# Performance work log

Measured on AMD Instinct MI355X. Metric: run time of the kernel, lower is better.

Reference implementation:

```python
import jax, jax.numpy as jnp
import numpy as np

N = 100000   # nodes per branch
E = 1600000  # edges per branch
B = 512      # graphs in batch
D = 256      # input feature dim
C = 27       # number of side-effect labels
NEG_SLOPE = 0.2


def _gat_conv(x, src, dst, W, a_src, a_dst, b):
    """PyG GATConv, heads=1, with self loops. x:[N,din], src/dst:[E+N]."""
    n = x.shape[0]
    h = x @ W                               # [N, dout]
    al_s = h @ a_src                        # [N]
    al_d = h @ a_dst                        # [N]
    e = jax.nn.leaky_relu(al_s[src] + al_d[dst], NEG_SLOPE)  # [E+N]
    # segment softmax over destination nodes (self loops guarantee non-empty)
    m = jax.ops.segment_max(e, dst, num_segments=n)
    w = jnp.exp(e - m[dst])
    denom = jax.ops.segment_sum(w, dst, num_segments=n)
    alpha = w / denom[dst]                  # [E+N]
    out = jax.ops.segment_sum(h[src] * alpha[:, None], dst, num_segments=n)
    return out + b


def _with_self_loops(edge_index, n):
    loop = jnp.arange(n, dtype=edge_index.dtype)
    src = jnp.concatenate([edge_index[0], loop])
    dst = jnp.concatenate([edge_index[1], loop])
    return src, dst


def _mean_pool(x, batch, num_graphs):
    s = jax.ops.segment_sum(x, batch, num_segments=num_graphs)
    cnt = jax.ops.segment_sum(jnp.ones(x.shape[0], x.dtype), batch, num_segments=num_graphs)
    return s / jnp.maximum(cnt, 1.0)[:, None]


def _gat_params(key, din, dout):
    k = jax.random.split(key, 4)
    sc = 1.0 / np.sqrt(din)
    return (jax.random.normal(k[0], (din, dout), jnp.float32) * sc,
            jax.random.normal(k[1], (dout,), jnp.float32) * sc,
            jax.random.normal(k[2], (dout,), jnp.float32) * sc,
            jnp.zeros((dout,), jnp.float32))


def setup_inputs() -> dict:
    key = jax.random.key(0)
    ks = jax.random.split(key, 12)
    inp = {
        'x_s': jax.random.normal(ks[0], (N, D), jnp.float32),
        'x_t': jax.random.normal(ks[1], (N, D), jnp.float32),
        'edge_index_s': jax.random.randint(ks[2], (2, E), 0, N, jnp.int32),
        'edge_index_t': jax.random.randint(ks[3], (2, E), 0, N, jnp.int32),
        'xs_batch': jnp.sort(jax.random.randint(ks[4], (N,), 0, B, jnp.int32)),
        'xt_batch': jnp.sort(jax.random.randint(ks[5], (N,), 0, B, jnp.int32)),
    }
    for name, kk, din, dout in [('s1', ks[6], D, D // 2), ('s2', ks[7], D // 2, D // 4),
                                 ('t1', ks[8], D, D // 2), ('t2', ks[9], D // 2, D // 4)]:
        W, a_s, a_d, b = _gat_params(kk, din, dout)
        inp[f'W_{name}'] = W
        inp[f'a_src_{name}'] = a_s
        inp[f'a_dst_{name}'] = a_d
        inp[f'b_{name}'] = b
    inp['lin_w'] = jax.random.normal(ks[10], (D // 4, C), jnp.float32) / np.sqrt(D // 4)
    inp['lin_b'] = jnp.zeros((C,), jnp.float32)
    return inp


def reference(x_s, x_t,
              W_s1, a_src_s1, a_dst_s1, b_s1,
              W_s2, a_src_s2, a_dst_s2, b_s2,
              W_t1, a_src_t1, a_dst_t1, b_t1,
              W_t2, a_src_t2, a_dst_t2, b_t2,
              lin_w, lin_b,
              edge_index_s, edge_index_t, xs_batch, xt_batch):
    src_s, dst_s = _with_self_loops(edge_index_s, N)
    src_t, dst_t = _with_self_loops(edge_index_t, N)

    x1 = _gat_conv(x_s, src_s, dst_s, W_s1, a_src_s1, a_dst_s1, b_s1)
    x2 = _gat_conv(x1, src_s, dst_s, W_s2, a_src_s2, a_dst_s2, b_s2)
    xs = _mean_pool(x2, xs_batch, B)

    x3 = _gat_conv(x_t, src_t, dst_t, W_t1, a_src_t1, a_dst_t1, b_t1)
    x4 = _gat_conv(x3, src_t, dst_t, W_t2, a_src_t2, a_dst_t2, b_t2)
    xt = _mean_pool(x4, xt_batch, B)

    out = (xs + xt) @ lin_w + lin_b        # [B, C]
    return jax.nn.sigmoid(out)
```

## Files before the change

kernel.cpp:

```cpp
#include <hip/hip_runtime.h>
#include <hip/hip_bf16.h>
#include <math.h>

#define NEG_SLOPE 0.2f

static const int NN = 100000;
static const int EE = 1600000;
static const int BB = 512;
static const int NTOT = 2 * NN;
static const int ETOT = 2 * EE;
static const int NBUK = (NTOT + 511) / 512;
static const int CHUNK = 4096;
static const int NBLK = (ETOT + CHUNK - 1) / CHUNK;
static const int GB = (NN + 63) / 64;

typedef __attribute__((ext_vector_type(8))) short bf16x8;
typedef __attribute__((ext_vector_type(4))) float f32x4;
typedef __attribute__((ext_vector_type(2))) float f32x2;

__device__ __forceinline__ float leaky(float x) { return x >= 0.f ? x : NEG_SLOPE * x; }

__device__ __forceinline__ unsigned short f2b(float f) {
    __hip_bfloat16 h = __float2bfloat16(f);
    return *reinterpret_cast<unsigned short*>(&h);
}
__device__ __forceinline__ float b2f_lo(unsigned v) { return __uint_as_float(v << 16); }
__device__ __forceinline__ float b2f_hi(unsigned v) { return __uint_as_float(v & 0xFFFF0000u); }
__device__ __forceinline__ unsigned packb(float a, float b) {
    return (unsigned)f2b(a) | ((unsigned)f2b(b) << 16);
}

__device__ __forceinline__ void pkfma(f32x2& acc, f32x2 h, f32x2 w) {
    asm("v_pk_fma_f32 %0, %1, %2, %0" : "+v"(acc) : "v"(h), "v"(w));
}
__device__ __forceinline__ f32x2 unpk(unsigned v) {
    f32x2 r;
    r.x = b2f_lo(v);
    r.y = b2f_hi(v);
    return r;
}

__device__ __forceinline__ void gload_lds16(const void* g, void* l) {
    __builtin_amdgcn_global_load_lds(
        (const __attribute__((address_space(1))) void*)g,
        (__attribute__((address_space(3))) void*)l, 16, 0, 0);
}

__global__ void wt2_kernel(const float* __restrict__ Ws, const float* __restrict__ Wt_,
                           unsigned short* __restrict__ WT, int K, int N) {
    int idx = blockIdx.x * blockDim.x + threadIdx.x;
    if (idx >= 2 * K * N) return;
    int br = idx >= K * N;
    int j = idx - br * K * N;
    int n = j / K, k = j - n * K;
    const float* W = br ? Wt_ : Ws;
    WT[idx] = f2b(W[(size_t)k * N + n]);
}

template <int K, int N, bool ABF>
__global__ __launch_bounds__(256, 3) void gemm_fused_kernel(
        const void* __restrict__ Av_s, const void* __restrict__ Av_t,
        const unsigned short* __restrict__ WT,
        const float* __restrict__ as_s, const float* __restrict__ ad_s,
        const float* __restrict__ as_t, const float* __restrict__ ad_t,
        unsigned* __restrict__ hb, float* __restrict__ al_s, float* __restrict__ al_d,
        int nblk) {
    constexpr int NT2 = N / 32;
    constexpr int ES = ABF ? 2 : 4;
    constexpr int ROWB = (K / 2) * ES;
    constexpr int CPR = ROWB / 16;
    constexpr int STB = 64 * ROWB;
    constexpr int IPW = (STB / 16) / 256;
    constexpr int SWZ = (CPR - 1) < 15 ? (CPR - 1) : 15;
    constexpr int KBH = (K / 2) / 32;

    __shared__ __align__(16) unsigned char Atile[STB];
    __shared__ float als0[64], ald0[64];

    const int bid = blockIdx.x;
    const int br = (bid >= nblk) ? 1 : 0;
    const int lb = bid - br * nblk;
    const int t = threadIdx.x;
    const int l = t & 63, w = t >> 6;
    const int wm = w >> 1, wn = w & 1;
    const int rl = l & 15, kh = l >> 4;
    const int row0blk = lb * 64;
    const char* Ab = (const char*)(br ? Av_t : Av_s);
    const unsigned short* WTb = WT + (size_t)br * N * K;
    const float* asv = br ? as_t : as_s;
    const float* adv = br ? ad_t : ad_s;

    f32x4 acc[2][NT2];
    #pragma unroll
    for (int g = 0; g < 2; g++)
        #pragma unroll
        for (int q = 0; q < NT2; q++) acc[g][q] = (f32x4){0.f, 0.f, 0.f, 0.f};

    #pragma unroll
    for (int h = 0; h < 2; h++) {
        #pragma unroll
        for (int i = 0; i < IPW; i++) {
            int c = (i * 4 + w) * 64 + l;
            int row = c / CPR, jp = c % CPR;
            int jg = jp ^ (row & SWZ);
            int rowg = min(row0blk + row, NN - 1);
            const char* src = Ab + ((size_t)rowg * K + h * (K / 2)) * ES + jg * 16;
            gload_lds16(src, Atile + c * 16);
        }
        bf16x8 Bv[KBH * NT2];
        #pragma unroll
        for (int kb = 0; kb < KBH; kb++)
            #pragma unroll
            for (int q = 0; q < NT2; q++) {
                int c = wn * (N / 2) + q * 16 + rl;
                Bv[kb * NT2 + q] =
                    *(const bf16x8*)(WTb + (size_t)c * K + h * (K / 2) + kb * 32 + kh * 8);
            }
        __syncthreads();
        #pragma unroll
        for (int kb = 0; kb < KBH; kb++) {
            bf16x8 av[2];
            #pragma unroll
            for (int rg = 0; rg < 2; rg++) {
                int r = wm * 32 + rg * 16 + rl;
                if constexpr (ABF) {
                    int j = kb * 4 + kh;
                    int js = j ^ (r & SWZ);
                    av[rg] = *(const bf16x8*)(Atile + r * ROWB + js * 16);
                } else {
                    int j0 = kb * 8 + kh * 2;
                    int j0s = j0 ^ (r & SWZ);
                    int j1s = (j0 + 1) ^ (r & SWZ);
                    float4 fa = *(const float4*)(Atile + r * ROWB + j0s * 16);
                    float4 fb = *(const float4*)(Atile + r * ROWB + j1s * 16);
                    union { bf16x8 v; unsigned short u[8]; } au;
                    au.u[0] = f2b(fa.x); au.u[1] = f2b(fa.y);
                    au.u[2] = f2b(fa.z); au.u[3] = f2b(fa.w);
                    au.u[4] = f2b(fb.x); au.u[5] = f2b(fb.y);
                    au.u[6] = f2b(fb.z); au.u[7] = f2b(fb.w);
                    av[rg] = au.v;
                }
            }
            #pragma unroll
            for (int q = 0; q < NT2; q++) {
                acc[0][q] = __builtin_amdgcn_mfma_f32_16x16x32_bf16(av[0], Bv[kb * NT2 + q], acc[0][q], 0, 0, 0);
                acc[1][q] = __builtin_amdgcn_mfma_f32_16x16x32_bf16(av[1], Bv[kb * NT2 + q], acc[1][q], 0, 0, 0);
            }
        }
        __syncthreads();
    }

    float asr[NT2], adr[NT2];
    #pragma unroll
    for (int q = 0; q < NT2; q++) {
        int c = wn * (N / 2) + q * 16 + rl;
        asr[q] = asv[c];
        adr[q] = adv[c];
    }

    float psA[2][4], pdA[2][4];
    #pragma unroll
    for (int rg = 0; rg < 2; rg++) {
        #pragma unroll
        for (int i = 0; i < 4; i++) {
            float ps = 0.f, pd = 0.f;
            #pragma unroll
            for (int q = 0; q < NT2; q++) {
                float v = acc[rg][q][i];
                ps += v * asr[q];
                pd += v * adr[q];
            }
            #pragma unroll
            for (int off = 1; off < 16; off <<= 1) {
                ps += __shfl_xor(ps, off);
                pd += __shfl_xor(pd, off);
            }
            psA[rg][i] = ps;
            pdA[rg][i] = pd;
        }
    }
    if (wn == 0 && rl == 0) {
        #pragma unroll
        for (int rg = 0; rg < 2; rg++)
            #pragma unroll
            for (int i = 0; i < 4; i++) {
                int rloc = wm * 32 + rg * 16 + kh * 4 + i;
                als0[rloc] = psA[rg][i];
                ald0[rloc] = pdA[rg][i];
            }
    }
    __syncthreads();
    if (wn == 1 && rl == 0) {
        #pragma unroll
        for (int rg = 0; rg < 2; rg++)
            #pragma unroll
            for (int i = 0; i < 4; i++) {
                int rloc = wm * 32 + rg * 16 + kh * 4 + i;
                int rlocal = lb * 64 + rloc;
                if (rlocal < NN) {
                    int g = br * NN + rlocal;
                    al_s[g] = psA[rg][i] + als0[rloc];
                    al_d[g] = pdA[rg][i] + ald0[rloc];
                }
            }
    }
    #pragma unroll
    for (int rg = 0; rg < 2; rg++) {
        #pragma unroll
        for (int i = 0; i < 4; i++) {
            int rlocal = lb * 64 + wm * 32 + rg * 16 + kh * 4 + i;
            bool ok = (rlocal < NN);
            int g = br * NN + rlocal;
            #pragma unroll
            for (int q = 0; q < NT2; q++) {
                float v = acc[rg][q][i];
                float hi = __shfl_xor(v, 1);
                if (ok && !(rl & 1)) {
                    int c = wn * (N / 2) + q * 16 + rl;
                    hb[(size_t)g * (N / 2) + (c >> 1)] = packb(v, hi);
                }
            }
        }
    }
}

__global__ __launch_bounds__(256) void bin_sort_kernel(const int* __restrict__ src_s,
                                                       const int* __restrict__ dst_s,
                                                       const int* __restrict__ src_t,
                                                       const int* __restrict__ dst_t,
                                                       uint2* __restrict__ region,
                                                       int* __restrict__ shist) {
    __shared__ int hist[512];
    __shared__ int part[256];
    __shared__ int cur[512];
    __shared__ uint2 lbuf[CHUNK];
    const int b = blockIdx.x, t = threadIdx.x;
    const int base = b * CHUNK;
    const int cnt = min(CHUNK, ETOT - base);
    hist[t] = 0; hist[t + 256] = 0;
    __syncthreads();
    unsigned es[16], ed[16];
    #pragma unroll
    for (int i = 0; i < 16; i++) {
        int li = i * 256 + t;
        if (li < cnt) {
            int e = base + li;
            if (e < EE) {
                es[i] = (unsigned)src_s[e];
                ed[i] = (unsigned)dst_s[e];
            } else {
                es[i] = (unsigned)src_t[e - EE] + NN;
                ed[i] = (unsigned)dst_t[e - EE] + NN;
            }
            atomicAdd(&hist[ed[i] >> 9], 1);
        }
    }
    __syncthreads();
    int d0 = hist[2 * t], d1 = hist[2 * t + 1];
    int s = d0 + d1;
    part[t] = s;
    __syncthreads();
    for (int off = 1; off < 256; off <<= 1) {
        int u = (t >= off) ? part[t - off] : 0;
        __syncthreads();
        part[t] += u;
        __syncthreads();
    }
    int ex = part[t] - s;
    cur[2 * t] = ex;
    cur[2 * t + 1] = ex + d0;
    if (2 * t < NBUK + 1) shist[(2 * t) * NBLK + b] = ex;
    if (2 * t + 1 < NBUK + 1) shist[(2 * t + 1) * NBLK + b] = ex + d0;
    __syncthreads();
    #pragma unroll
    for (int i = 0; i < 16; i++) {
        int li = i * 256 + t;
        if (li < cnt) {
            int slot = atomicAdd(&cur[ed[i] >> 9], 1);
            lbuf[slot] = make_uint2(es[i], ed[i]);
        }
    }
    __syncthreads();
    for (int i = t; i < cnt; i += 256) region[base + i] = lbuf[i];
}

__global__ void bucket_tot_kernel(const int* __restrict__ shist, int* __restrict__ btot) {
    __shared__ int red[256];
    const int k = blockIdx.x, t = threadIdx.x;
    int s = 0;
    for (int b = t; b < NBLK; b += 256)
        s += shist[(k + 1) * NBLK + b] - shist[k * NBLK + b];
    red[t] = s;
    __syncthreads();
    for (int off = 128; off > 0; off >>= 1) {
        if (t < off) red[t] += red[t + off];
        __syncthreads();
    }
    if (t == 0) btot[k] = red[0];
}

__global__ void bucket_scan_kernel(const int* __restrict__ btot, int* __restrict__ bbase) {
    __shared__ int part[256];
    int t = threadIdx.x;
    int v0 = (2 * t < NBUK) ? btot[2 * t] : 0;
    int v1 = (2 * t + 1 < NBUK) ? btot[2 * t + 1] : 0;
    int s = v0 + v1;
    part[t] = s;
    __syncthreads();
    for (int off = 1; off < 256; off <<= 1) {
        int u = (t >= off) ? part[t - off] : 0;
        __syncthreads();
        part[t] += u;
        __syncthreads();
    }
    int ex = part[t] - s;
    if (2 * t < NBUK) bbase[2 * t] = ex;
    if (2 * t + 1 < NBUK) bbase[2 * t + 1] = ex + v0;
}

__global__ __launch_bounds__(256) void csr_bucket_kernel(const uint2* __restrict__ region,
                                                         const int* __restrict__ shist,
                                                         const int* __restrict__ bbase,
                                                         int* __restrict__ rowptr,
                                                         int* __restrict__ col) {
    __shared__ int deg[512];
    __shared__ int part[256];
    __shared__ int cur[512];
    const int k = blockIdx.x, t = threadIdx.x;
    const int n0 = k * 512;
    const int nloc = min(512, NTOT - n0);
    const int base = bbase[k];
    deg[t] = 0; deg[t + 256] = 0;
    __syncthreads();
    for (int b = t; b < NBLK; b += 256) {
        int s0 = shist[k * NBLK + b], s1 = shist[(k + 1) * NBLK + b];
        for (int i = s0; i < s1; i++) {
            uint2 e = region[(size_t)b * CHUNK + i];
            atomicAdd(&deg[(int)e.y - n0], 1);
        }
    }
    __syncthreads();
    int d0 = deg[2 * t], d1 = deg[2 * t + 1];
    int s = d0 + d1;
    part[t] = s;
    __syncthreads();
    for (int off = 1; off < 256; off <<= 1) {
        int u = (t >= off) ? part[t - off] : 0;
        __syncthreads();
        part[t] += u;
        __syncthreads();
    }
    int ex = part[t] - s;
    cur[2 * t] = ex;
    cur[2 * t + 1] = ex + d0;
    if (2 * t < nloc) rowptr[n0 + 2 * t] = base + ex;
    if (2 * t + 1 < nloc) rowptr[n0 + 2 * t + 1] = base + ex + d0;
    if (t == 0 && n0 + nloc == NTOT) rowptr[NTOT] = base + part[255];
    __syncthreads();
    for (int b = t; b < NBLK; b += 256) {
        int s0 = shist[k * NBLK + b], s1 = shist[(k + 1) * NBLK + b];
        for (int i = s0; i < s1; i++) {
            uint2 e = region[(size_t)b * CHUNK + i];
            int pos = atomicAdd(&cur[(int)e.y - n0], 1);
            col[base + pos] = (int)e.x;
        }
    }
}

__global__ void brow2_kernel(const int* __restrict__ bs, const int* __restrict__ bt,
                             int* __restrict__ brow_s, int* __restrict__ brow_t) {
    int g = blockIdx.x * blockDim.x + threadIdx.x;
    const int* batch;
    int* brow;
    int gg;
    if (g <= BB) { batch = bs; brow = brow_s; gg = g; }
    else if (g <= 2 * BB + 1) { batch = bt; brow = brow_t; gg = g - (BB + 1); }
    else return;
    int lo = 0, hi = NN;
    while (lo < hi) {
        int mid = (lo + hi) >> 1;
        if (batch[mid] < gg) lo = mid + 1; else hi = mid;
    }
    brow[gg] = lo;
}

__global__ void gat_gather128_kernel(const int* __restrict__ rowptr, const int* __restrict__ col,
                                     const float* __restrict__ al_s, const float* __restrict__ al_d,
                                     const unsigned* __restrict__ hb,
                                     const float* __restrict__ bias_s,
                                     const float* __restrict__ bias_t,
                                     unsigned* __restrict__ outb) {
    int node = blockIdx.x * 4 + (threadIdx.x >> 6);
    int lane = threadIdx.x & 63;
    if (node >= NTOT) return;
    const float* bias = (node < NN) ? bias_s : bias_t;
    const int slot = lane >> 4, sub = lane & 15;
    const int beg = rowptr[node], end = rowptr[node + 1];
    const float ald = al_d[node];
    const float e_self = leaky(al_s[node] + ald);

    f32x2 acc2[4];
    #pragma unroll
    for (int k = 0; k < 4; k++) acc2[k] = (f32x2){0.f, 0.f};
    float dsum = 0.f;
    for (int base = beg; base < end; base += 64) {
        int i = base + lane;
        float w = 0.f; int s = 0;
        if (i < end) {
            s = col[i];
            w = expf(leaky(al_s[s] + ald));
        }
        dsum += w;
        int cnt = min(64, end - base);
        for (int j = 0; j < cnt; j += 8) {
            int idx0 = j + slot, idx1 = j + 4 + slot;
            float w0 = __shfl(w, idx0), w1 = __shfl(w, idx1);
            int s0 = __shfl(s, idx0), s1 = __shfl(s, idx1);
            uint4 v0 = *(const uint4*)(hb + (size_t)s0 * 64 + sub * 4);
            uint4 v1 = *(const uint4*)(hb + (size_t)s1 * 64 + sub * 4);
            f32x2 wp0 = (f32x2){w0, w0}, wp1 = (f32x2){w1, w1};
            pkfma(acc2[0], unpk(v0.x), wp0);
            pkfma(acc2[1], unpk(v0.y), wp0);
            pkfma(acc2[2], unpk(v0.z), wp0);
            pkfma(acc2[3], unpk(v0.w), wp0);
            pkfma(acc2[0], unpk(v1.x), wp1);
            pkfma(acc2[1], unpk(v1.y), wp1);
            pkfma(acc2[2], unpk(v1.z), wp1);
            pkfma(acc2[3], unpk(v1.w), wp1);
        }
    }
    float acc[8];
    #pragma unroll
    for (int k = 0; k < 4; k++) { acc[2 * k] = acc2[k].x; acc[2 * k + 1] = acc2[k].y; }
    #pragma unroll
    for (int k = 0; k < 8; k++) {
        acc[k] += __shfl_xor(acc[k], 16);
        acc[k] += __shfl_xor(acc[k], 32);
    }
    #pragma unroll
    for (int off = 32; off > 0; off >>= 1) dsum += __shfl_xor(dsum, off);

    float wself = expf(e_self);
    dsum += wself;
    float inv = 1.f / dsum;
    if (slot == 0) {
        uint4 sv = *(const uint4*)(hb + (size_t)node * 64 + sub * 4);
        float sf[8] = { b2f_lo(sv.x), b2f_hi(sv.x), b2f_lo(sv.y), b2f_hi(sv.y),
                        b2f_lo(sv.z), b2f_hi(sv.z), b2f_lo(sv.w), b2f_hi(sv.w) };
        float o[8];
        #pragma unroll
        for (int k = 0; k < 8; k++)
            o[k] = bias[sub * 8 + k] + (acc[k] + wself * sf[k]) * inv;
        uint4 r = make_uint4(packb(o[0], o[1]), packb(o[2], o[3]),
                             packb(o[4], o[5]), packb(o[6], o[7]));
        *(uint4*)(outb + (size_t)node * 64 + sub * 4) = r;
    }
}

__global__ void gat_gather64_kernel(const int* __restrict__ rowptr, const int* __restrict__ col,
                                    const float* __restrict__ al_s, const float* __restrict__ al_d,
                                    const unsigned* __restrict__ hb,
                                    const float* __restrict__ bias_s,
                                    const float* __restrict__ bias_t,
                                    float* __restrict__ out) {
    int node = blockIdx.x * 4 + (threadIdx.x >> 6);
    int lane = threadIdx.x & 63;
    if (node >= NTOT) return;
    const float* bias = (node < NN) ? bias_s : bias_t;
    const int slot = lane >> 4, sub = lane & 15;
    const int beg = rowptr[node], end = rowptr[node + 1];
    const float ald = al_d[node];
    const float e_self = leaky(al_s[node] + ald);

    f32x2 acc2[2];
    acc2[0] = (f32x2){0.f, 0.f};
    acc2[1] = (f32x2){0.f, 0.f};
    float dsum = 0.f;
    for (int base = beg; base < end; base += 64) {
        int i = base + lane;
        float w = 0.f; int s = 0;
        if (i < end) {
            s = col[i];
            w = expf(leaky(al_s[s] + ald));
        }
        dsum += w;
        int cnt = min(64, end - base);
        for (int j = 0; j < cnt; j += 8) {
            int idx0 = j + slot, idx1 = j + 4 + slot;
            float w0 = __shfl(w, idx0), w1 = __shfl(w, idx1);
            int s0 = __shfl(s, idx0), s1 = __shfl(s, idx1);
            uint2 v0 = *(const uint2*)(hb + (size_t)s0 * 32 + sub * 2);
            uint2 v1 = *(const uint2*)(hb + (size_t)s1 * 32 + sub * 2);
            f32x2 wp0 = (f32x2){w0, w0}, wp1 = (f32x2){w1, w1};
            pkfma(acc2[0], unpk(v0.x), wp0);
            pkfma(acc2[1], unpk(v0.y), wp0);
            pkfma(acc2[0], unpk(v1.x), wp1);
            pkfma(acc2[1], unpk(v1.y), wp1);
        }
    }
    float acc[4] = { acc2[0].x, acc2[0].y, acc2[1].x, acc2[1].y };
    #pragma unroll
    for (int k = 0; k < 4; k++) {
        acc[k] += __shfl_xor(acc[k], 16);
        acc[k] += __shfl_xor(acc[k], 32);
    }
    #pragma unroll
    for (int off = 32; off > 0; off >>= 1) dsum += __shfl_xor(dsum, off);

    float wself = expf(e_self);
    dsum += wself;
    float inv = 1.f / dsum;
    if (slot == 0) {
        uint2 sv = *(const uint2*)(hb + (size_t)node * 32 + sub * 2);
        float sf[4] = { b2f_lo(sv.x), b2f_hi(sv.x), b2f_lo(sv.y), b2f_hi(sv.y) };
        float4 o;
        o.x = bias[sub * 4 + 0] + (acc[0] + wself * sf[0]) * inv;
        o.y = bias[sub * 4 + 1] + (acc[1] + wself * sf[1]) * inv;
        o.z = bias[sub * 4 + 2] + (acc[2] + wself * sf[2]) * inv;
        o.w = bias[sub * 4 + 3] + (acc[3] + wself * sf[3]) * inv;
        *(float4*)(out + (size_t)node * 64 + sub * 4) = o;
    }
}

__global__ void pool_seg_kernel(const float* __restrict__ x,
                                const int* __restrict__ brow_s, const int* __restrict__ brow_t,
                                float* __restrict__ pooled_s, float* __restrict__ pooled_t) {
    __shared__ float red[4][64];
    int g = blockIdx.x;
    int tb = g >= BB;
    int gb = g - tb * BB;
    const int* brow = tb ? brow_t : brow_s;
    float* pooled = tb ? pooled_t : pooled_s;
    int off = tb ? NN : 0;
    int lane = threadIdx.x & 63, w = threadIdx.x >> 6;
    int beg = brow[gb], end = brow[gb + 1];
    float acc = 0.f;
    for (int n = beg + w; n < end; n += 4)
        acc += x[(size_t)(off + n) * 64 + lane];
    red[w][lane] = acc;
    __syncthreads();
    if (w == 0) {
        float s = red[0][lane] + red[1][lane] + red[2][lane] + red[3][lane];
        float cnt = (float)(end - beg);
        pooled[(size_t)gb * 64 + lane] = s / fmaxf(cnt, 1.f);
    }
}

__global__ void final_kernel(const float* __restrict__ ps, const float* __restrict__ pt,
                             const float* __restrict__ lw, const float* __restrict__ lb,
                             float* __restrict__ out) {
    int g = blockIdx.x;
    int c = threadIdx.x;
    if (c >= 27) return;
    float acc = lb[c];
    #pragma unroll 8
    for (int k = 0; k < 64; k++) {
        float xv = ps[g * 64 + k] + pt[g * 64 + k];
        acc += xv * lw[k * 27 + c];
    }
    out[g * 27 + c] = 1.f / (1.f + expf(-acc));
}

extern "C" void kernel_launch(void* const* d_in, const int* in_sizes, int n_in,
                              void* d_out, int out_size, void* d_ws, size_t ws_size,
                              hipStream_t stream) {
    const float* x_s = (const float*)d_in[0];
    const float* x_t = (const float*)d_in[1];
    const int* ei_s = (const int*)d_in[2];
    const int* ei_t = (const int*)d_in[3];
    const int* xs_batch = (const int*)d_in[4];
    const int* xt_batch = (const int*)d_in[5];
    const float* W_s1 = (const float*)d_in[6];
    const float* a_src_s1 = (const float*)d_in[7];
    const float* a_dst_s1 = (const float*)d_in[8];
    const float* b_s1 = (const float*)d_in[9];
    const float* W_s2 = (const float*)d_in[10];
    const float* a_src_s2 = (const float*)d_in[11];
    const float* a_dst_s2 = (const float*)d_in[12];
    const float* b_s2 = (const float*)d_in[13];
    const float* W_t1 = (const float*)d_in[14];
    const float* a_src_t1 = (const float*)d_in[15];
    const float* a_dst_t1 = (const float*)d_in[16];
    const float* b_t1 = (const float*)d_in[17];
    const float* W_t2 = (const float*)d_in[18];
    const float* a_src_t2 = (const float*)d_in[19];
    const float* a_dst_t2 = (const float*)d_in[20];
    const float* b_t2 = (const float*)d_in[21];
    const float* lin_w = (const float*)d_in[22];
    const float* lin_b = (const float*)d_in[23];
    float* out = (float*)d_out;

    unsigned* hb = (unsigned*)d_ws;
    uint2* region = (uint2*)d_ws;
    unsigned* out1b = hb + (size_t)NTOT * 64;
    float* out2 = (float*)out1b;
    int* col = (int*)(out1b + (size_t)NTOT * 64);
    float* al_s = (float*)(col + ETOT);
    float* al_d = al_s + NTOT;
    float* pooled_s = al_d + NTOT;
    float* pooled_t = pooled_s + (size_t)BB * 64;
    unsigned short* WT1 = (unsigned short*)(pooled_t + (size_t)BB * 64);
    unsigned short* WT2 = WT1 + 2 * 256 * 128;
    int* rowptr = (int*)(WT2 + 2 * 128 * 64);
    int* shist = rowptr + NTOT + 1;
    int* btot = shist + (NBUK + 1) * NBLK;
    int* bbase = btot + NBUK;
    int* brow_s = bbase + NBUK;
    int* brow_t = brow_s + BB + 1;

    const int* src_s = ei_s;
    const int* dst_s = ei_s + EE;
    const int* src_t = ei_t;
    const int* dst_t = ei_t + EE;

    bin_sort_kernel<<<NBLK, 256, 0, stream>>>(src_s, dst_s, src_t, dst_t, region, shist);
    bucket_tot_kernel<<<NBUK, 256, 0, stream>>>(shist, btot);
    bucket_scan_kernel<<<1, 256, 0, stream>>>(btot, bbase);
    csr_bucket_kernel<<<NBUK, 256, 0, stream>>>(region, shist, bbase, rowptr, col);

    wt2_kernel<<<(2 * 256 * 128 + 255) / 256, 256, 0, stream>>>(W_s1, W_t1, WT1, 256, 128);
    gemm_fused_kernel<256, 128, false><<<2 * GB, 256, 0, stream>>>(
        x_s, x_t, WT1, a_src_s1, a_dst_s1, a_src_t1, a_dst_t1, hb, al_s, al_d, GB);
    gat_gather128_kernel<<<(NTOT + 3) / 4, 256, 0, stream>>>(
        rowptr, col, al_s, al_d, hb, b_s1, b_t1, out1b);

    wt2_kernel<<<(2 * 128 * 64 + 255) / 256, 256, 0, stream>>>(W_s2, W_t2, WT2, 128, 64);
    gemm_fused_kernel<128, 64, true><<<2 * GB, 256, 0, stream>>>(
        out1b, (const unsigned short*)out1b + (size_t)NN * 128, WT2,
        a_src_s2, a_dst_s2, a_src_t2, a_dst_t2, hb, al_s, al_d, GB);
    gat_gather64_kernel<<<(NTOT + 3) / 4, 256, 0, stream>>>(
        rowptr, col, al_s, al_d, hb, b_s2, b_t2, out2);

    brow2_kernel<<<(2 * (BB + 1) + 255) / 256, 256, 0, stream>>>(xs_batch, xt_batch, brow_s, brow_t);
    pool_seg_kernel<<<2 * BB, 256, 0, stream>>>(out2, brow_s, brow_t, pooled_s, pooled_t);
    final_kernel<<<BB, 32, 0, stream>>>(pooled_s, pooled_t, lin_w, lin_b, out);
}
```

Baseline: 458.2 us.

## Merge edge binning with first GEMM and fold small launch kernels

Runs the edge bin-sort and the layer-1 GEMM as disjoint block ranges of a single launch, so the two independent stages overlap and one launch is saved. To allow this, the sort region moves out of the hb workspace into its own buffer. Both weight transposes now happen in one kernel, and the graph-boundary binary search moves into the pooling kernel, removing two more launches. The costs are a larger shared-memory footprint for the merged kernel (38 KB for every block), which may lower occupancy for the binning blocks, and redundant binary searches in the pooling blocks.

```diff
diff --git a/kernel.cpp b/kernel.cpp
--- a/kernel.cpp
+++ b/kernel.cpp
@@ -29,7 +29,6 @@
 __device__ __forceinline__ unsigned packb(float a, float b) {
     return (unsigned)f2b(a) | ((unsigned)f2b(b) << 16);
 }
-
 __device__ __forceinline__ void pkfma(f32x2& acc, f32x2 h, f32x2 w) {
     asm("v_pk_fma_f32 %0, %1, %2, %0" : "+v"(acc) : "v"(h), "v"(w));
 }
@@ -46,195 +45,37 @@
         (__attribute__((address_space(3))) void*)l, 16, 0, 0);
 }
 
-__global__ void wt2_kernel(const float* __restrict__ Ws, const float* __restrict__ Wt_,
-                           unsigned short* __restrict__ WT, int K, int N) {
+__global__ void wt_all_kernel(const float* __restrict__ Ws1, const float* __restrict__ Wt1,
+                              const float* __restrict__ Ws2, const float* __restrict__ Wt2_,
+                              unsigned short* __restrict__ WT1, unsigned short* __restrict__ WT2) {
     int idx = blockIdx.x * blockDim.x + threadIdx.x;
-    if (idx >= 2 * K * N) return;
-    int br = idx >= K * N;
-    int j = idx - br * K * N;
-    int n = j / K, k = j - n * K;
-    const float* W = br ? Wt_ : Ws;
-    WT[idx] = f2b(W[(size_t)k * N + n]);
-}
-
-template <int K, int N, bool ABF>
-__global__ __launch_bounds__(256, 3) void gemm_fused_kernel(
-        const void* __restrict__ Av_s, const void* __restrict__ Av_t,
-        const unsigned short* __restrict__ WT,
-        const float* __restrict__ as_s, const float* __restrict__ ad_s,
-        const float* __restrict__ as_t, const float* __restrict__ ad_t,
-        unsigned* __restrict__ hb, float* __restrict__ al_s, float* __restrict__ al_d,
-        int nblk) {
-    constexpr int NT2 = N / 32;
-    constexpr int ES = ABF ? 2 : 4;
-    constexpr int ROWB = (K / 2) * ES;
-    constexpr int CPR = ROWB / 16;
-    constexpr int STB = 64 * ROWB;
-    constexpr int IPW = (STB / 16) / 256;
-    constexpr int SWZ = (CPR - 1) < 15 ? (CPR - 1) : 15;
-    constexpr int KBH = (K / 2) / 32;
-
-    __shared__ __align__(16) unsigned char Atile[STB];
-    __shared__ float als0[64], ald0[64];
-
-    const int bid = blockIdx.x;
-    const int br = (bid >= nblk) ? 1 : 0;
-    const int lb = bid - br * nblk;
+    if (idx < 2 * 256 * 128) {
+        int br = idx >= 256 * 128;
+        int j = idx - br * 256 * 128;
+        int n = j / 256, k = j - n * 256;
+        const float* W = br ? Wt1 : Ws1;
+        WT1[idx] = f2b(W[(size_t)k * 128 + n]);
+    } else {
+        int x = idx - 2 * 256 * 128;
+        if (x >= 2 * 128 * 64) return;
+        int br = x >= 128 * 64;
+        int j = x - br * 128 * 64;
+        int n = j / 128, k = j - n * 128;
+        const float* W = br ? Wt2_ : Ws2;
+        WT2[x] = f2b(W[(size_t)k * 64 + n]);
+    }
+}
+
+
+__device__ __forceinline__ void bin_body(int b, unsigned char* smem,
+                                         const int* __restrict__ src_s, const int* __restrict__ dst_s,
+                                         const int* __restrict__ src_t, const int* __restrict__ dst_t,
+                                         uint2* __restrict__ region, int* __restrict__ shist) {
+    int* hist = (int*)smem;
+    int* part = hist + 512;
+    int* cur = part + 256;
+    uint2* lbuf = (uint2*)(smem + 5120);
     const int t = threadIdx.x;
-    const int l = t & 63, w = t >> 6;
-    const int wm = w >> 1, wn = w & 1;
-    const int rl = l & 15, kh = l >> 4;
-    const int row0blk = lb * 64;
-    const char* Ab = (const char*)(br ? Av_t : Av_s);
-    const unsigned short* WTb = WT + (size_t)br * N * K;
-    const float* asv = br ? as_t : as_s;
-    const float* adv = br ? ad_t : ad_s;
-
-    f32x4 acc[2][NT2];
-    #pragma unroll
-    for (int g = 0; g < 2; g++)
-        #pragma unroll
-        for (int q = 0; q < NT2; q++) acc[g][q] = (f32x4){0.f, 0.f, 0.f, 0.f};
-
-    #pragma unroll
-    for (int h = 0; h < 2; h++) {
-        #pragma unroll
-        for (int i = 0; i < IPW; i++) {
-            int c = (i * 4 + w) * 64 + l;
-            int row = c / CPR, jp = c % CPR;
-            int jg = jp ^ (row & SWZ);
-            int rowg = min(row0blk + row, NN - 1);
-            const char* src = Ab + ((size_t)rowg * K + h * (K / 2)) * ES + jg * 16;
-            gload_lds16(src, Atile + c * 16);
-        }
-        bf16x8 Bv[KBH * NT2];
-        #pragma unroll
-        for (int kb = 0; kb < KBH; kb++)
-            #pragma unroll
-            for (int q = 0; q < NT2; q++) {
-                int c = wn * (N / 2) + q * 16 + rl;
-                Bv[kb * NT2 + q] =
-                    *(const bf16x8*)(WTb + (size_t)c * K + h * (K / 2) + kb * 32 + kh * 8);
-            }
-        __syncthreads();
-        #pragma unroll
-        for (int kb = 0; kb < KBH; kb++) {
-            bf16x8 av[2];
-            #pragma unroll
-            for (int rg = 0; rg < 2; rg++) {
-                int r = wm * 32 + rg * 16 + rl;
-                if constexpr (ABF) {
-                    int j = kb * 4 + kh;
-                    int js = j ^ (r & SWZ);
-                    av[rg] = *(const bf16x8*)(Atile + r * ROWB + js * 16);
-                } else {
-                    int j0 = kb * 8 + kh * 2;
-                    int j0s = j0 ^ (r & SWZ);
-                    int j1s = (j0 + 1) ^ (r & SWZ);
-                    float4 fa = *(const float4*)(Atile + r * ROWB + j0s * 16);
-                    float4 fb = *(const float4*)(Atile + r * ROWB + j1s * 16);
-                    union { bf16x8 v; unsigned short u[8]; } au;
-                    au.u[0] = f2b(fa.x); au.u[1] = f2b(fa.y);
-                    au.u[2] = f2b(fa.z); au.u[3] = f2b(fa.w);
-                    au.u[4] = f2b(fb.x); au.u[5] = f2b(fb.y);
-                    au.u[6] = f2b(fb.z); au.u[7] = f2b(fb.w);
-                    av[rg] = au.v;
-                }
-            }
-            #pragma unroll
-            for (int q = 0; q < NT2; q++) {
-                acc[0][q] = __builtin_amdgcn_mfma_f32_16x16x32_bf16(av[0], Bv[kb * NT2 + q], acc[0][q], 0, 0, 0);
-                acc[1][q] = __builtin_amdgcn_mfma_f32_16x16x32_bf16(av[1], Bv[kb * NT2 + q], acc[1][q], 0, 0, 0);
-            }
-        }
-        __syncthreads();
-    }
-
-    float asr[NT2], adr[NT2];
-    #pragma unroll
-    for (int q = 0; q < NT2; q++) {
-        int c = wn * (N / 2) + q * 16 + rl;
-        asr[q] = asv[c];
-        adr[q] = adv[c];
-    }
-
-    float psA[2][4], pdA[2][4];
-    #pragma unroll
-    for (int rg = 0; rg < 2; rg++) {
-        #pragma unroll
-        for (int i = 0; i < 4; i++) {
-            float ps = 0.f, pd = 0.f;
-            #pragma unroll
-            for (int q = 0; q < NT2; q++) {
-                float v = acc[rg][q][i];
-                ps += v * asr[q];
-                pd += v * adr[q];
-            }
-            #pragma unroll
-            for (int off = 1; off < 16; off <<= 1) {
-                ps += __shfl_xor(ps, off);
-                pd += __shfl_xor(pd, off);
-            }
-            psA[rg][i] = ps;
-            pdA[rg][i] = pd;
-        }
-    }
-    if (wn == 0 && rl == 0) {
-        #pragma unroll
-        for (int rg = 0; rg < 2; rg++)
-            #pragma unroll
-            for (int i = 0; i < 4; i++) {
-                int rloc = wm * 32 + rg * 16 + kh * 4 + i;
-                als0[rloc] = psA[rg][i];
-                ald0[rloc] = pdA[rg][i];
-            }
-    }
-    __syncthreads();
-    if (wn == 1 && rl == 0) {
-        #pragma unroll
-        for (int rg = 0; rg < 2; rg++)
-            #pragma unroll
-            for (int i = 0; i < 4; i++) {
-                int rloc = wm * 32 + rg * 16 + kh * 4 + i;
-                int rlocal = lb * 64 + rloc;
-                if (rlocal < NN) {
-                    int g = br * NN + rlocal;
-                    al_s[g] = psA[rg][i] + als0[rloc];
-                    al_d[g] = pdA[rg][i] + ald0[rloc];
-                }
-            }
-    }
-    #pragma unroll
-    for (int rg = 0; rg < 2; rg++) {
-        #pragma unroll
-        for (int i = 0; i < 4; i++) {
-            int rlocal = lb * 64 + wm * 32 + rg * 16 + kh * 4 + i;
-            bool ok = (rlocal < NN);
-            int g = br * NN + rlocal;
-            #pragma unroll
-            for (int q = 0; q < NT2; q++) {
-                float v = acc[rg][q][i];
-                float hi = __shfl_xor(v, 1);
-                if (ok && !(rl & 1)) {
-                    int c = wn * (N / 2) + q * 16 + rl;
-                    hb[(size_t)g * (N / 2) + (c >> 1)] = packb(v, hi);
-                }
-            }
-        }
-    }
-}
-
-__global__ __launch_bounds__(256) void bin_sort_kernel(const int* __restrict__ src_s,
-                                                       const int* __restrict__ dst_s,
-                                                       const int* __restrict__ src_t,
-                                                       const int* __restrict__ dst_t,
-                                                       uint2* __restrict__ region,
-                                                       int* __restrict__ shist) {
-    __shared__ int hist[512];
-    __shared__ int part[256];
-    __shared__ int cur[512];
-    __shared__ uint2 lbuf[CHUNK];
-    const int b = blockIdx.x, t = threadIdx.x;
     const int base = b * CHUNK;
     const int cnt = min(CHUNK, ETOT - base);
     hist[t] = 0; hist[t + 256] = 0;
@@ -282,6 +123,335 @@
     }
     __syncthreads();
     for (int i = t; i < cnt; i += 256) region[base + i] = lbuf[i];
+}
+
+__device__ __forceinline__ void gemm1_body(int bid, unsigned char* smem,
+                                           const float* __restrict__ Av_s, const float* __restrict__ Av_t,
+                                           const unsigned short* __restrict__ WT,
+                                           const float* __restrict__ as_s, const float* __restrict__ ad_s,
+                                           const float* __restrict__ as_t, const float* __restrict__ ad_t,
+                                           unsigned* __restrict__ hb,
+                                           float* __restrict__ al_s, float* __restrict__ al_d) {
+    constexpr int K = 256, N = 128;
+    constexpr int NT2 = 4;
+    constexpr int ROWB = 512;
+    constexpr int CPR = 32;
+    constexpr int IPW = 8;
+    constexpr int SWZ = 15;
+    constexpr int KBH = 4;
+
+    unsigned char* Atile = smem;
+    float* als0 = (float*)(smem + 32768);
+    float* ald0 = als0 + 64;
+
+    const int br = (bid >= GB) ? 1 : 0;
+    const int lb = bid - br * GB;
+    const int t = threadIdx.x;
+    const int l = t & 63, w = t >> 6;
+    const int wm = w >> 1, wn = w & 1;
+    const int rl = l & 15, kh = l >> 4;
+    const int row0blk = lb * 64;
+    const char* Ab = (const char*)(br ? Av_t : Av_s);
+    const unsigned short* WTb = WT + (size_t)br * N * K;
+    const float* asv = br ? as_t : as_s;
+    const float* adv = br ? ad_t : ad_s;
+
+    f32x4 acc[2][NT2];
+    #pragma unroll
+    for (int g = 0; g < 2; g++)
+        #pragma unroll
+        for (int q = 0; q < NT2; q++) acc[g][q] = (f32x4){0.f, 0.f, 0.f, 0.f};
+
+    #pragma unroll
+    for (int h = 0; h < 2; h++) {
+        #pragma unroll
+        for (int i = 0; i < IPW; i++) {
+            int c = (i * 4 + w) * 64 + l;
+            int row = c / CPR, jp = c % CPR;
+            int jg = jp ^ (row & SWZ);
+            int rowg = min(row0blk + row, NN - 1);
+            const char* src = Ab + ((size_t)rowg * K + h * (K / 2)) * 4 + jg * 16;
+            gload_lds16(src, Atile + c * 16);
+        }
+        bf16x8 Bv[KBH * NT2];
+        #pragma unroll
+        for (int kb = 0; kb < KBH; kb++)
+            #pragma unroll
+            for (int q = 0; q < NT2; q++) {
+                int c = wn * (N / 2) + q * 16 + rl;
+                Bv[kb * NT2 + q] =
+                    *(const bf16x8*)(WTb + (size_t)c * K + h * (K / 2) + kb * 32 + kh * 8);
+            }
+        __syncthreads();
+        #pragma unroll
+        for (int kb = 0; kb < KBH; kb++) {
+            bf16x8 av[2];
+            #pragma unroll
+            for (int rg = 0; rg < 2; rg++) {
+                int r = wm * 32 + rg * 16 + rl;
+                int j0 = kb * 8 + kh * 2;
+                int j0s = j0 ^ (r & SWZ);
+                int j1s = (j0 + 1) ^ (r & SWZ);
+                float4 fa = *(const float4*)(Atile + r * ROWB + j0s * 16);
+                float4 fb = *(const float4*)(Atile + r * ROWB + j1s * 16);
+                union { bf16x8 v; unsigned short u[8]; } au;
+                au.u[0] = f2b(fa.x); au.u[1] = f2b(fa.y);
+                au.u[2] = f2b(fa.z); au.u[3] = f2b(fa.w);
+                au.u[4] = f2b(fb.x); au.u[5] = f2b(fb.y);
+                au.u[6] = f2b(fb.z); au.u[7] = f2b(fb.w);
+                av[rg] = au.v;
+            }
+            #pragma unroll
+            for (int q = 0; q < NT2; q++) {
+                acc[0][q] = __builtin_amdgcn_mfma_f32_16x16x32_bf16(av[0], Bv[kb * NT2 + q], acc[0][q], 0, 0, 0);
+                acc[1][q] = __builtin_amdgcn_mfma_f32_16x16x32_bf16(av[1], Bv[kb * NT2 + q], acc[1][q], 0, 0, 0);
+            }
+        }
+        __syncthreads();
+    }
+
+    float asr[NT2], adr[NT2];
+    #pragma unroll
+    for (int q = 0; q < NT2; q++) {
+        int c = wn * (N / 2) + q * 16 + rl;
+        asr[q] = asv[c];
+        adr[q] = adv[c];
+    }
+
+    float psA[2][4], pdA[2][4];
+    #pragma unroll
+    for (int rg = 0; rg < 2; rg++) {
+        #pragma unroll
+        for (int i = 0; i < 4; i++) {
+            float ps = 0.f, pd = 0.f;
+            #pragma unroll
+            for (int q = 0; q < NT2; q++) {
+                float v = acc[rg][q][i];
+                ps += v * asr[q];
+                pd += v * adr[q];
+            }
+            #pragma unroll
+            for (int off = 1; off < 16; off <<= 1) {
+                ps += __shfl_xor(ps, off);
+                pd += __shfl_xor(pd, off);
+            }
+            psA[rg][i] = ps;
+            pdA[rg][i] = pd;
+        }
+    }
+    if (wn == 0 && rl == 0) {
+        #pragma unroll
+        for (int rg = 0; rg < 2; rg++)
+            #pragma unroll
+            for (int i = 0; i < 4; i++) {
+                int rloc = wm * 32 + rg * 16 + kh * 4 + i;
+                als0[rloc] = psA[rg][i];
+                ald0[rloc] = pdA[rg][i];
+            }
+    }
+    __syncthreads();
+    if (wn == 1 && rl == 0) {
+        #pragma unroll
+        for (int rg = 0; rg < 2; rg++)
+            #pragma unroll
+            for (int i = 0; i < 4; i++) {
+                int rloc = wm * 32 + rg * 16 + kh * 4 + i;
+                int rlocal = lb * 64 + rloc;
+                if (rlocal < NN) {
+                    int g = br * NN + rlocal;
+                    al_s[g] = psA[rg][i] + als0[rloc];
+                    al_d[g] = pdA[rg][i] + ald0[rloc];
+                }
+            }
+    }
+    #pragma unroll
+    for (int rg = 0; rg < 2; rg++) {
+        #pragma unroll
+        for (int i = 0; i < 4; i++) {
+            int rlocal = lb * 64 + wm * 32 + rg * 16 + kh * 4 + i;
+            bool ok = (rlocal < NN);
+            int g = br * NN + rlocal;
+            #pragma unroll
+            for (int q = 0; q < NT2; q++) {
+                float v = acc[rg][q][i];
+                float hi = __shfl_xor(v, 1);
+                if (ok && !(rl & 1)) {
+                    int c = wn * (N / 2) + q * 16 + rl;
+                    hb[(size_t)g * (N / 2) + (c >> 1)] = packb(v, hi);
+                }
+            }
+        }
+    }
+}
+
+__global__ __launch_bounds__(256, 3) void gemm1_bin_kernel(
+        const float* __restrict__ Av_s, const float* __restrict__ Av_t,
+        const unsigned short* __restrict__ WT,
+        const float* __restrict__ as_s, const float* __restrict__ ad_s,
+        const float* __restrict__ as_t, const float* __restrict__ ad_t,
+        unsigned* __restrict__ hb, float* __restrict__ al_s, float* __restrict__ al_d,
+        const int* __restrict__ src_s, const int* __restrict__ dst_s,
+        const int* __restrict__ src_t, const int* __restrict__ dst_t,
+        uint2* __restrict__ region, int* __restrict__ shist) {
+    __shared__ __align__(16) unsigned char smem[38912];
+    int bid = blockIdx.x;
+    if (bid < NBLK) {
+        bin_body(bid, smem, src_s, dst_s, src_t, dst_t, region, shist);
+    } else {
+        gemm1_body(bid - NBLK, smem, Av_s, Av_t, WT, as_s, ad_s, as_t, ad_t, hb, al_s, al_d);
+    }
+}
+
+template <int K, int N>
+__global__ __launch_bounds__(256, 3) void gemm2_kernel(
+        const unsigned short* __restrict__ Ab_s, const unsigned short* __restrict__ Ab_t,
+        const unsigned short* __restrict__ WT,
+        const float* __restrict__ as_s, const float* __restrict__ ad_s,
+        const float* __restrict__ as_t, const float* __restrict__ ad_t,
+        unsigned* __restrict__ hb, float* __restrict__ al_s, float* __restrict__ al_d,
+        int nblk) {
+    constexpr int NT2 = N / 32;
+    constexpr int ROWB = (K / 2) * 2;
+    constexpr int CPR = ROWB / 16;
+    constexpr int STB = 64 * ROWB;
+    constexpr int IPW = (STB / 16) / 256;
+    constexpr int SWZ = (CPR - 1) < 15 ? (CPR - 1) : 15;
+    constexpr int KBH = (K / 2) / 32;
+
+    __shared__ __align__(16) unsigned char Atile[STB];
+    __shared__ float als0[64], ald0[64];
+
+    const int bid = blockIdx.x;
+    const int br = (bid >= nblk) ? 1 : 0;
+    const int lb = bid - br * nblk;
+    const int t = threadIdx.x;
+    const int l = t & 63, w = t >> 6;
+    const int wm = w >> 1, wn = w & 1;
+    const int rl = l & 15, kh = l >> 4;
+    const int row0blk = lb * 64;
+    const char* Ab = (const char*)(br ? Ab_t : Ab_s);
+    const unsigned short* WTb = WT + (size_t)br * N * K;
+    const float* asv = br ? as_t : as_s;
+    const float* adv = br ? ad_t : ad_s;
+
+    f32x4 acc[2][NT2];
+    #pragma unroll
+    for (int g = 0; g < 2; g++)
+        #pragma unroll
+        for (int q = 0; q < NT2; q++) acc[g][q] = (f32x4){0.f, 0.f, 0.f, 0.f};
+
+    #pragma unroll
+    for (int h = 0; h < 2; h++) {
+        #pragma unroll
+        for (int i = 0; i < IPW; i++) {
+            int c = (i * 4 + w) * 64 + l;
+            int row = c / CPR, jp = c % CPR;
+            int jg = jp ^ (row & SWZ);
+            int rowg = min(row0blk + row, NN - 1);
+            const char* src = Ab + ((size_t)rowg * K + h * (K / 2)) * 2 + jg * 16;
+            gload_lds16(src, Atile + c * 16);
+        }
+        bf16x8 Bv[KBH * NT2];
+        #pragma unroll
+        for (int kb = 0; kb < KBH; kb++)
+            #pragma unroll
+            for (int q = 0; q < NT2; q++) {
+                int c = wn * (N / 2) + q * 16 + rl;
+                Bv[kb * NT2 + q] =
+                    *(const bf16x8*)(WTb + (size_t)c * K + h * (K / 2) + kb * 32 + kh * 8);
+            }
+        __syncthreads();
+        #pragma unroll
+        for (int kb = 0; kb < KBH; kb++) {
+            bf16x8 av[2];
+            #pragma unroll
+            for (int rg = 0; rg < 2; rg++) {
+                int r = wm * 32 + rg * 16 + rl;
+                int j = kb * 4 + kh;
+                int js = j ^ (r & SWZ);
+                av[rg] = *(const bf16x8*)(Atile + r * ROWB + js * 16);
+            }
+            #pragma unroll
+            for (int q = 0; q < NT2; q++) {
+                acc[0][q] = __builtin_amdgcn_mfma_f32_16x16x32_bf16(av[0], Bv[kb * NT2 + q], acc[0][q], 0, 0, 0);
+                acc[1][q] = __builtin_amdgcn_mfma_f32_16x16x32_bf16(av[1], Bv[kb * NT2 + q], acc[1][q], 0, 0, 0);
+            }
+        }
+        __syncthreads();
+    }
+
+    float asr[NT2], adr[NT2];
+    #pragma unroll
+    for (int q = 0; q < NT2; q++) {
+        int c = wn * (N / 2) + q * 16 + rl;
+        asr[q] = asv[c];
+        adr[q] = adv[c];
+    }
+
+    float psA[2][4], pdA[2][4];
+    #pragma unroll
+    for (int rg = 0; rg < 2; rg++) {
+        #pragma unroll
+        for (int i = 0; i < 4; i++) {
+            float ps = 0.f, pd = 0.f;
+            #pragma unroll
+            for (int q = 0; q < NT2; q++) {
+                float v = acc[rg][q][i];
+                ps += v * asr[q];
+                pd += v * adr[q];
+            }
+            #pragma unroll
+            for (int off = 1; off < 16; off <<= 1) {
+                ps += __shfl_xor(ps, off);
+                pd += __shfl_xor(pd, off);
+            }
+            psA[rg][i] = ps;
+            pdA[rg][i] = pd;
+        }
+    }
+    if (wn == 0 && rl == 0) {
+        #pragma unroll
+        for (int rg = 0; rg < 2; rg++)
+            #pragma unroll
+            for (int i = 0; i < 4; i++) {
+                int rloc = wm * 32 + rg * 16 + kh * 4 + i;
+                als0[rloc] = psA[rg][i];
+                ald0[rloc] = pdA[rg][i];
+            }
+    }
+    __syncthreads();
+    if (wn == 1 && rl == 0) {
+        #pragma unroll
+        for (int rg = 0; rg < 2; rg++)
+            #pragma unroll
+            for (int i = 0; i < 4; i++) {
+                int rloc = wm * 32 + rg * 16 + kh * 4 + i;
+                int rlocal = lb * 64 + rloc;
+                if (rlocal < NN) {
+                    int g = br * NN + rlocal;
+                    al_s[g] = psA[rg][i] + als0[rloc];
+                    al_d[g] = pdA[rg][i] + ald0[rloc];
+                }
+            }
+    }
+    #pragma unroll
+    for (int rg = 0; rg < 2; rg++) {
+        #pragma unroll
+        for (int i = 0; i < 4; i++) {
+            int rlocal = lb * 64 + wm * 32 + rg * 16 + kh * 4 + i;
+            bool ok = (rlocal < NN);
+            int g = br * NN + rlocal;
+            #pragma unroll
+            for (int q = 0; q < NT2; q++) {
+                float v = acc[rg][q][i];
+                float hi = __shfl_xor(v, 1);
+                if (ok && !(rl & 1)) {
+                    int c = wn * (N / 2) + q * 16 + rl;
+                    hb[(size_t)g * (N / 2) + (c >> 1)] = packb(v, hi);
+                }
+            }
+        }
+    }
 }
 
 __global__ void bucket_tot_kernel(const int* __restrict__ shist, int* __restrict__ btot) {
@@ -365,23 +535,6 @@
             col[base + pos] = (int)e.x;
         }
     }
-}
-
-__global__ void brow2_kernel(const int* __restrict__ bs, const int* __restrict__ bt,
-                             int* __restrict__ brow_s, int* __restrict__ brow_t) {
-    int g = blockIdx.x * blockDim.x + threadIdx.x;
-    const int* batch;
-    int* brow;
-    int gg;
-    if (g <= BB) { batch = bs; brow = brow_s; gg = g; }
-    else if (g <= 2 * BB + 1) { batch = bt; brow = brow_t; gg = g - (BB + 1); }
-    else return;
-    int lo = 0, hi = NN;
-    while (lo < hi) {
-        int mid = (lo + hi) >> 1;
-        if (batch[mid] < gg) lo = mid + 1; else hi = mid;
-    }
-    brow[gg] = lo;
 }
 
 __global__ void gat_gather128_kernel(const int* __restrict__ rowptr, const int* __restrict__ col,
@@ -523,17 +676,28 @@
 }
 
 __global__ void pool_seg_kernel(const float* __restrict__ x,
-                                const int* __restrict__ brow_s, const int* __restrict__ brow_t,
+                                const int* __restrict__ bs, const int* __restrict__ bt,
                                 float* __restrict__ pooled_s, float* __restrict__ pooled_t) {
     __shared__ float red[4][64];
+    __shared__ int bnd[2];
     int g = blockIdx.x;
     int tb = g >= BB;
     int gb = g - tb * BB;
-    const int* brow = tb ? brow_t : brow_s;
+    const int* batch = tb ? bt : bs;
     float* pooled = tb ? pooled_t : pooled_s;
     int off = tb ? NN : 0;
+    if (threadIdx.x < 2) {
+        int target = gb + threadIdx.x;
+        int lo = 0, hi = NN;
+        while (lo < hi) {
+            int mid = (lo + hi) >> 1;
+            if (batch[mid] < target) lo = mid + 1; else hi = mid;
+        }
+        bnd[threadIdx.x] = lo;
+    }
+    __syncthreads();
+    int beg = bnd[0], end = bnd[1];
     int lane = threadIdx.x & 63, w = threadIdx.x >> 6;
-    int beg = brow[gb], end = brow[gb + 1];
     float acc = 0.f;
     for (int n = beg + w; n < end; n += 4)
         acc += x[(size_t)(off + n) * 64 + lane];
@@ -591,10 +755,10 @@
     float* out = (float*)d_out;
 
     unsigned* hb = (unsigned*)d_ws;
-    uint2* region = (uint2*)d_ws;
     unsigned* out1b = hb + (size_t)NTOT * 64;
     float* out2 = (float*)out1b;
-    int* col = (int*)(out1b + (size_t)NTOT * 64);
+    uint2* region = (uint2*)(out1b + (size_t)NTOT * 64);
+    int* col = (int*)(region + (size_t)NBLK * CHUNK);
     float* al_s = (float*)(col + ETOT);
     float* al_d = al_s + NTOT;
     float* pooled_s = al_d + NTOT;
@@ -605,33 +769,32 @@
     int* shist = rowptr + NTOT + 1;
     int* btot = shist + (NBUK + 1) * NBLK;
     int* bbase = btot + NBUK;
-    int* brow_s = bbase + NBUK;
-    int* brow_t = brow_s + BB + 1;
 
     const int* src_s = ei_s;
     const int* dst_s = ei_s + EE;
     const int* src_t = ei_t;
     const int* dst_t = ei_t + EE;
 
-    bin_sort_kernel<<<NBLK, 256, 0, stream>>>(src_s, dst_s, src_t, dst_t, region, shist);
+    wt_all_kernel<<<(2 * 256 * 128 + 2 * 128 * 64 + 255) / 256, 256, 0, stream>>>(
+        W_s1, W_t1, W_s2, W_t2, WT1, WT2);
+
+    gemm1_bin_kernel<<<NBLK + 2 * GB, 256, 0, stream>>>(
+        x_s, x_t, WT1, a_src_s1, a_dst_s1, a_src_t1, a_dst_t1, hb, al_s, al_d,
+        src_s, dst_s, src_t, dst_t, region, shist);
+
     bucket_tot_kernel<<<NBUK, 256, 0, stream>>>(shist, btot);
     bucket_scan_kernel<<<1, 256, 0, stream>>>(btot, bbase);
     csr_bucket_kernel<<<NBUK, 256, 0, stream>>>(region, shist, bbase, rowptr, col);
 
-    wt2_kernel<<<(2 * 256 * 128 + 255) / 256, 256, 0, stream>>>(W_s1, W_t1, WT1, 256, 128);
-    gemm_fused_kernel<256, 128, false><<<2 * GB, 256, 0, stream>>>(
-        x_s, x_t, WT1, a_src_s1, a_dst_s1, a_src_t1, a_dst_t1, hb, al_s, al_d, GB);
     gat_gather128_kernel<<<(NTOT + 3) / 4, 256, 0, stream>>>(
         rowptr, col, al_s, al_d, hb, b_s1, b_t1, out1b);
 
-    wt2_kernel<<<(2 * 128 * 64 + 255) / 256, 256, 0, stream>>>(W_s2, W_t2, WT2, 128, 64);
-    gemm_fused_kernel<128, 64, true><<<2 * GB, 256, 0, stream>>>(
-        out1b, (const unsigned short*)out1b + (size_t)NN * 128, WT2,
+    gemm2_kernel<128, 64><<<2 * GB, 256, 0, stream>>>(
+        (const unsigned short*)out1b, (const unsigned short*)out1b + (size_t)NN * 128, WT2,
         a_src_s2, a_dst_s2, a_src_t2, a_dst_t2, hb, al_s, al_d, GB);
     gat_gather64_kernel<<<(NTOT + 3) / 4, 256, 0, stream>>>(
         rowptr, col, al_s, al_d, hb, b_s2, b_t2, out2);
 
-    brow2_kernel<<<(2 * (BB + 1) + 255) / 256, 256, 0, stream>>>(xs_batch, xt_batch, brow_s, brow_t);
-    pool_seg_kernel<<<2 * BB, 256, 0, stream>>>(out2, brow_s, brow_t, pooled_s, pooled_t);
+    pool_seg_kernel<<<2 * BB, 256, 0, stream>>>(out2, xs_batch, xt_batch, pooled_s, pooled_t);
     final_kernel<<<BB, 32, 0, stream>>>(pooled_s, pooled_t, lin_w, lin_b, out);
 }
```

After: 451.3 us. No clear change (-1.5%).
